# Kernel optimization log

Hardware: AMD Instinct MI355X
Metric: run time of the kernel (lower is better)

Reference implementation:

```python
import jax, jax.numpy as jnp
import numpy as np

HEAD_DIM = 256
V_DIM = 256
HIDDEN = 1024
SCALE_BASE = 512
GAMMA = 0.96875
BATCH, SEQ = 4, 4096


def _dup_interleave(m):
    # (L, d/2) -> (L, d), duplicating each column consecutively
    return jnp.repeat(m, 2, axis=-1)


def _rotate_every_two(x):
    x1 = x[..., ::2]
    x2 = x[..., 1::2]
    return jnp.stack([-x2, x1], axis=-1).reshape(x.shape)


def _xpos(x, downscale=False):
    # x: (B, L, head_dim); offset=0 path of XPOS.forward
    B, L, Dh = x.shape
    half = Dh // 2
    scale_buf = (jnp.arange(0, Dh, 2, dtype=jnp.float32) + 0.4 * Dh) / (1.4 * Dh)  # (half,)
    pos = jnpp = jnp.arange(L, dtype=jnp.float32)
    scale = scale_buf[None, :] ** (pos / SCALE_BASE)[:, None]  # (L, half)
    inv_freq = 1.0 / (10000.0 ** (jnp.arange(half, dtype=jnp.float32) / half))
    sinusoid = pos[:, None] * inv_freq[None, :]  # (L, half)
    sin, cos = jnp.sin(sinusoid), jnp.cos(sinusoid)
    if downscale:
        scale = 1.0 / scale
    cos_s = _dup_interleave(cos * scale)  # (L, Dh)
    sin_s = _dup_interleave(sin * scale)
    return x * cos_s[None] + _rotate_every_two(x) * sin_s[None]


def _decay_matrix(L):
    n = jnp.arange(L)[:, None]
    m = jnp.arange(L)[None, :]
    mask = n >= m
    expo = jnp.where(mask, n - m, 0).astype(jnp.float32)
    return jnp.where(mask, GAMMA ** expo, 0.0)  # (L, L)


def setup_inputs() -> dict:
    key = jax.random.key(0)
    k1, k2, k3, k4 = jax.random.split(key, 4)
    X = jax.random.normal(k1, (BATCH, SEQ, HIDDEN), dtype=jnp.float32)
    W_Q = jax.random.normal(k2, (HIDDEN, HEAD_DIM), dtype=jnp.float32) / HIDDEN
    W_K = jax.random.normal(k3, (HIDDEN, HEAD_DIM), dtype=jnp.float32) / HIDDEN
    W_V = jax.random.normal(k4, (HIDDEN, V_DIM), dtype=jnp.float32) / HIDDEN
    return {"X": X, "W_Q": W_Q, "W_K": W_K, "W_V": W_V}


def reference(X, W_Q, W_K, W_V):
    L = X.shape[1]
    Q = _xpos(X @ W_Q)                      # (B, L, Dh)
    K = _xpos(X @ W_K, downscale=True)      # (B, L, Dh)
    V = X @ W_V                             # (B, L, Dv)
    D = _decay_matrix(L)                    # (L, L)
    ret = jnp.einsum('bqd,bkd->bqk', Q, K) * D[None]  # (B, L, L)
    return ret @ V                          # (B, L, Dv)
```

## Files before the change

### kernel.cpp

```cpp
#include <hip/hip_runtime.h>
#include <hip/hip_bf16.h>
#include <cstdint>
#include <cstddef>

#define L_SEQ 4096
#define BATCH_N 4
#define HID 1024
#define DH 256
#define LOG2_GAMMA (-0.045803689613124953f)

typedef __attribute__((ext_vector_type(8))) short short8;
typedef __attribute__((ext_vector_type(4))) float floatx4;

__device__ __forceinline__ unsigned short f2bf(float f) {
    union { float f; unsigned int u; } v; v.f = f;
    unsigned int r = (v.u + 0x7FFFu + ((v.u >> 16) & 1u)) >> 16;
    return (unsigned short)r;
}

__device__ __forceinline__ void async_copy16(const unsigned short* gsrc,
                                             unsigned short* lds) {
    __builtin_amdgcn_global_load_lds(
        (const __attribute__((address_space(1))) unsigned int*)gsrc,
        (__attribute__((address_space(3))) unsigned int*)lds, 16, 0, 0);
}

__global__ __launch_bounds__(256) void convert_x_kernel(
    const float* __restrict__ X, unsigned short* __restrict__ Xb)
{
    const int i = (blockIdx.x * 256 + threadIdx.x) * 4;
    const float4 v = *(const float4*)&X[i];
    ushort4 p;
    p.x = f2bf(v.x); p.y = f2bf(v.y); p.z = f2bf(v.z); p.w = f2bf(v.w);
    *(ushort4*)&Xb[i] = p;
}

__global__ __launch_bounds__(256) void transpose_w_kernel(
    const float* __restrict__ WQ, const float* __restrict__ WK,
    const float* __restrict__ WV, unsigned short* __restrict__ Wt)
{
    __shared__ float Ts[64][68];
    const int n0 = blockIdx.x * 64;
    const int k0 = blockIdx.y * 64;
    const int seg = n0 >> 8;
    const float* __restrict__ W = (seg == 0) ? WQ : (seg == 1) ? WK : WV;
    const int nl0 = n0 & 255;

    const int t  = threadIdx.x;
    const int r  = t >> 4;
    const int c4 = (t & 15) * 4;
    #pragma unroll
    for (int i = 0; i < 4; ++i) {
        const int kk = r + i * 16;
        const float4 v = *(const float4*)&W[(size_t)(k0 + kk) * DH + nl0 + c4];
        Ts[c4 + 0][kk] = v.x;
        Ts[c4 + 1][kk] = v.y;
        Ts[c4 + 2][kk] = v.z;
        Ts[c4 + 3][kk] = v.w;
    }
    __syncthreads();
    const int rn = t >> 3;
    const int c8 = (t & 7) * 8;
    #pragma unroll
    for (int i = 0; i < 2; ++i) {
        const int rr = rn + i * 32;
        ushort4 p0, p1;
        p0.x = f2bf(Ts[rr][c8 + 0]); p0.y = f2bf(Ts[rr][c8 + 1]);
        p0.z = f2bf(Ts[rr][c8 + 2]); p0.w = f2bf(Ts[rr][c8 + 3]);
        p1.x = f2bf(Ts[rr][c8 + 4]); p1.y = f2bf(Ts[rr][c8 + 5]);
        p1.z = f2bf(Ts[rr][c8 + 6]); p1.w = f2bf(Ts[rr][c8 + 7]);
        unsigned short* dst = &Wt[(size_t)(n0 + rr) * HID + k0 + c8];
        *(ushort4*)dst       = p0;
        *(ushort4*)(dst + 4) = p1;
    }
}

__global__ __launch_bounds__(256) void gemm_qkv_kernel(
    const unsigned short* __restrict__ Wt,
    const unsigned short* __restrict__ Xb,
    unsigned short* __restrict__ Qo,
    unsigned short* __restrict__ Ko,
    unsigned short* __restrict__ VtG)
{
    __shared__ unsigned short Wa[128][32];
    __shared__ unsigned short Xs[128][32];

    const int n0 = blockIdx.x * 128;
    const int p0 = blockIdx.y * 128;
    const int t    = threadIdx.x;
    const int w    = t >> 6;
    const int lane = t & 63;
    const int quad = lane >> 4;
    const int l16  = lane & 15;
    const int wn   = (w & 1) * 64;
    const int wp   = (w >> 1) * 64;

    const int srow = w * 32 + (lane >> 2);
    const int scol = (lane & 3) * 8;

    floatx4 acc[4][4];
    #pragma unroll
    for (int i = 0; i < 4; ++i)
        #pragma unroll
        for (int j = 0; j < 4; ++j) acc[i][j] = (floatx4){0.f, 0.f, 0.f, 0.f};

    for (int k0 = 0; k0 < HID; k0 += 32) {
        __syncthreads();
        #pragma unroll
        for (int is = 0; is < 2; ++is) {
            const unsigned short* ga =
                &Wt[(size_t)(n0 + srow + is * 16) * HID + k0 + scol];
            const unsigned short* gb =
                &Xb[(size_t)(p0 + srow + is * 16) * HID + k0 + scol];
            async_copy16(ga, &Wa[w * 32 + is * 16][0]);
            async_copy16(gb, &Xs[w * 32 + is * 16][0]);
        }
        __syncthreads();

        short8 af[4], bf[4];
        #pragma unroll
        for (int nt = 0; nt < 4; ++nt)
            af[nt] = *(const short8*)&Wa[wn + nt * 16 + l16][quad * 8];
        #pragma unroll
        for (int pt = 0; pt < 4; ++pt)
            bf[pt] = *(const short8*)&Xs[wp + pt * 16 + l16][quad * 8];
        #pragma unroll
        for (int nt = 0; nt < 4; ++nt)
            #pragma unroll
            for (int pt = 0; pt < 4; ++pt)
                acc[nt][pt] = __builtin_amdgcn_mfma_f32_16x16x32_bf16(
                    af[nt], bf[pt], acc[nt][pt], 0, 0, 0);
    }

    const int seg = n0 >> 8;
    #pragma unroll
    for (int nt = 0; nt < 4; ++nt) {
        const int nfeat = n0 + wn + nt * 16 + quad * 4;
        const int d0 = nfeat & 255;
        #pragma unroll
        for (int pt = 0; pt < 4; ++pt) {
            const int pg  = p0 + wp + pt * 16 + l16;
            const int b   = pg >> 12;
            const int pos = pg & (L_SEQ - 1);
            if (seg == 2) {
                #pragma unroll
                for (int g = 0; g < 4; ++g)
                    VtG[(((size_t)(b * 256 + d0 + g)) << 12) + pos] =
                        f2bf(acc[nt][pt][g]);
            } else {
                const float e = (float)pos * (1.0f / 512.0f);
                float res[4];
                #pragma unroll
                for (int h = 0; h < 4; h += 2) {
                    const int d  = d0 + h;
                    const int i2 = d >> 1;
                    const float sb = ((float)d + 102.4f) * (1.0f / 358.4f);
                    float sc = exp2f(log2f(sb) * e);
                    if (seg == 1) sc = 1.0f / sc;
                    const float invf = exp2f(-13.287712379549449f *
                                             ((float)i2 * (1.0f / 128.0f)));
                    float s, c;
                    sincosf((float)pos * invf, &s, &c);
                    const float cs = c * sc, ss = s * sc;
                    const float xe = acc[nt][pt][h], xo = acc[nt][pt][h + 1];
                    res[h]     = xe * cs - xo * ss;
                    res[h + 1] = xo * cs + xe * ss;
                }
                ushort4 pk;
                pk.x = f2bf(res[0]); pk.y = f2bf(res[1]);
                pk.z = f2bf(res[2]); pk.w = f2bf(res[3]);
                unsigned short* orow =
                    ((seg == 0) ? Qo : Ko) + (size_t)pg * DH + d0;
                *(ushort4*)orow = pk;
            }
        }
    }
}

__global__ __launch_bounds__(256) void retention_kernel(
    const unsigned short* __restrict__ Q,
    const unsigned short* __restrict__ K,
    const unsigned short* __restrict__ VtG,
    float* __restrict__ O)
{
    __shared__ short Qs[64][264];
    __shared__ short Ks[32][264];
    __shared__ short Vt[256][40];
    __shared__ short Ss[64][40];

    const int qt = blockIdx.x;
    const int b  = blockIdx.y;
    const int t  = threadIdx.x;
    const int q0 = qt * 64;

    const int w    = t >> 6;
    const int lane = t & 63;
    const int quad = lane >> 4;
    const int l16  = lane & 15;
    const int w16  = w * 16;

    const size_t rbase = (size_t)b * L_SEQ * DH;
    const size_t vbase = ((size_t)b * DH) << 12;

    {
        const unsigned short* src = Q + rbase + (size_t)q0 * DH;
        #pragma unroll
        for (int i = 0; i < 8; ++i) {
            const int row = i * 8 + (t >> 5);
            const int col = (t & 31) * 8;
            *(uint4*)&Qs[row][col] = *(const uint4*)&src[row * DH + col];
        }
    }

    floatx4 o[16];
    #pragma unroll
    for (int f = 0; f < 16; ++f) o[f] = (floatx4){0.f, 0.f, 0.f, 0.f};

    int kstart = q0 - 512;
    if (kstart < 0) kstart = 0;

    for (int k0 = kstart; k0 < q0 + 64; k0 += 32) {
        __syncthreads();
        {
            const unsigned short* src = K + rbase + (size_t)k0 * DH;
            #pragma unroll
            for (int i = 0; i < 4; ++i) {
                const int row = i * 8 + (t >> 5);
                const int col = (t & 31) * 8;
                *(uint4*)&Ks[row][col] = *(const uint4*)&src[row * DH + col];
            }
        }
        {
            const int koff = (t & 7) * 4;
            #pragma unroll
            for (int i = 0; i < 8; ++i) {
                const int c = (t >> 3) + 32 * i;
                *(uint2*)&Vt[c][koff] =
                    *(const uint2*)&VtG[vbase + ((size_t)c << 12) + k0 + koff];
            }
        }
        __syncthreads();

        #pragma unroll
        for (int ntile = 0; ntile < 2; ++ntile) {
            floatx4 s = (floatx4){0.f, 0.f, 0.f, 0.f};
            #pragma unroll
            for (int d8 = 0; d8 < 8; ++d8) {
                const short8 a   = *(const short8*)&Qs[w16 + l16][d8 * 32 + quad * 8];
                const short8 bfr = *(const short8*)&Ks[ntile * 16 + l16][d8 * 32 + quad * 8];
                s = __builtin_amdgcn_mfma_f32_16x16x32_bf16(a, bfr, s, 0, 0, 0);
            }
            const int kpos = k0 + ntile * 16 + l16;
            #pragma unroll
            for (int g = 0; g < 4; ++g) {
                const int qpos = q0 + w16 + quad * 4 + g;
                const int d = qpos - kpos;
                const float p = (d >= 0) ? s[g] * exp2f((float)d * LOG2_GAMMA) : 0.0f;
                Ss[w16 + quad * 4 + g][ntile * 16 + l16] = (short)f2bf(p);
            }
        }
        __syncthreads();

        {
            const short8 a = *(const short8*)&Ss[w16 + l16][quad * 8];
            #pragma unroll
            for (int f = 0; f < 16; ++f) {
                const short8 bfr = *(const short8*)&Vt[f * 16 + l16][quad * 8];
                o[f] = __builtin_amdgcn_mfma_f32_16x16x32_bf16(a, bfr, o[f], 0, 0, 0);
            }
        }
    }

    #pragma unroll
    for (int f = 0; f < 16; ++f) {
        #pragma unroll
        for (int g = 0; g < 4; ++g) {
            const int qpos = q0 + w16 + quad * 4 + g;
            O[rbase + (size_t)qpos * DH + f * 16 + l16] = o[f][g];
        }
    }
}

extern "C" void kernel_launch(void* const* d_in, const int* in_sizes, int n_in,
                              void* d_out, int out_size, void* d_ws, size_t ws_size,
                              hipStream_t stream)
{
    const float* X  = (const float*)d_in[0];
    const float* WQ = (const float*)d_in[1];
    const float* WK = (const float*)d_in[2];
    const float* WV = (const float*)d_in[3];
    float* out = (float*)d_out;

    const size_t per = (size_t)BATCH_N * L_SEQ * DH;
    unsigned short* Qw  = (unsigned short*)d_ws;
    unsigned short* Kw  = Qw + per;
    unsigned short* Vtw = Kw + per;
    unsigned short* Xbw = Vtw + per;
    unsigned short* Wtw = Xbw + (size_t)16384 * HID;

    convert_x_kernel<<<16384, 256, 0, stream>>>(X, Xbw);
    transpose_w_kernel<<<dim3(12, 16), 256, 0, stream>>>(WQ, WK, WV, Wtw);

    gemm_qkv_kernel<<<dim3(6, 128), 256, 0, stream>>>(Wtw, Xbw, Qw, Kw, Vtw);

    retention_kernel<<<dim3(L_SEQ / 64, BATCH_N), 256, 0, stream>>>(Qw, Kw, Vtw, out);
}
```

Measured before the change: 190.6 us.

## Fuse X bf16 conversion into QKV GEMM, remap blocks, retile retention kernel

```diff
diff --git a/kernel.cpp b/kernel.cpp
--- a/kernel.cpp
+++ b/kernel.cpp
@@ -25,15 +25,6 @@
         (__attribute__((address_space(3))) unsigned int*)lds, 16, 0, 0);
 }
 
-__global__ __launch_bounds__(256) void convert_x_kernel(
-    const float* __restrict__ X, unsigned short* __restrict__ Xb)
-{
-    const int i = (blockIdx.x * 256 + threadIdx.x) * 4;
-    const float4 v = *(const float4*)&X[i];
-    ushort4 p;
-    p.x = f2bf(v.x); p.y = f2bf(v.y); p.z = f2bf(v.z); p.w = f2bf(v.w);
-    *(ushort4*)&Xb[i] = p;
-}
 
 __global__ __launch_bounds__(256) void transpose_w_kernel(
     const float* __restrict__ WQ, const float* __restrict__ WK,
@@ -75,18 +66,22 @@
     }
 }
 
-__global__ __launch_bounds__(256) void gemm_qkv_kernel(
+__global__ __launch_bounds__(256, 3) void gemm_qkv_kernel(
     const unsigned short* __restrict__ Wt,
-    const unsigned short* __restrict__ Xb,
+    const float* __restrict__ X,
     unsigned short* __restrict__ Qo,
     unsigned short* __restrict__ Ko,
     unsigned short* __restrict__ VtG)
 {
-    __shared__ unsigned short Wa[128][32];
-    __shared__ unsigned short Xs[128][32];
-
-    const int n0 = blockIdx.x * 128;
-    const int p0 = blockIdx.y * 128;
+    __shared__ unsigned short Wa[2][128][32];
+    __shared__ unsigned short Xs[2][128][32];
+
+    const int idx = blockIdx.x;
+    const int xcd = idx & 7;
+    const int j   = idx >> 3;
+    const int n0  = (j % 6) * 128;
+    const int p0  = (xcd * 16 + (j / 6)) * 128;
+
     const int t    = threadIdx.x;
     const int w    = t >> 6;
     const int lane = t & 63;
@@ -95,41 +90,67 @@
     const int wn   = (w & 1) * 64;
     const int wp   = (w >> 1) * 64;
 
-    const int srow = w * 32 + (lane >> 2);
-    const int scol = (lane & 3) * 8;
+    const int arow = lane >> 2;
+    const int acol = (lane & 3) * 8;
+
+    const int rb = t >> 1;
+    const int hb = t & 1;
 
     floatx4 acc[4][4];
     #pragma unroll
     for (int i = 0; i < 4; ++i)
         #pragma unroll
-        for (int j = 0; j < 4; ++j) acc[i][j] = (floatx4){0.f, 0.f, 0.f, 0.f};
-
-    for (int k0 = 0; k0 < HID; k0 += 32) {
-        __syncthreads();
-        #pragma unroll
-        for (int is = 0; is < 2; ++is) {
+        for (int jj = 0; jj < 4; ++jj) acc[i][jj] = (floatx4){0.f, 0.f, 0.f, 0.f};
+
+    const float* xsrc0 = &X[(size_t)(p0 + rb) * HID + hb * 32];
+
+    for (int k0 = 0; k0 < HID; k0 += 64) {
+        float4 xv[8];
+        #pragma unroll
+        for (int i = 0; i < 8; ++i)
+            xv[i] = ((const float4*)(xsrc0 + k0))[i];
+
+        __syncthreads();
+
+        #pragma unroll
+        for (int s = 0; s < 4; ++s) {
+            const int panel = s & 1;
+            const int rch   = w * 32 + (s >> 1) * 16;
             const unsigned short* ga =
-                &Wt[(size_t)(n0 + srow + is * 16) * HID + k0 + scol];
-            const unsigned short* gb =
-                &Xb[(size_t)(p0 + srow + is * 16) * HID + k0 + scol];
-            async_copy16(ga, &Wa[w * 32 + is * 16][0]);
-            async_copy16(gb, &Xs[w * 32 + is * 16][0]);
-        }
-        __syncthreads();
-
-        short8 af[4], bf[4];
-        #pragma unroll
-        for (int nt = 0; nt < 4; ++nt)
-            af[nt] = *(const short8*)&Wa[wn + nt * 16 + l16][quad * 8];
-        #pragma unroll
-        for (int pt = 0; pt < 4; ++pt)
-            bf[pt] = *(const short8*)&Xs[wp + pt * 16 + l16][quad * 8];
-        #pragma unroll
-        for (int nt = 0; nt < 4; ++nt)
+                &Wt[(size_t)(n0 + rch + arow) * HID + k0 + panel * 32 + acol];
+            async_copy16(ga, &Wa[panel][rch][0]);
+        }
+        {
+            unsigned short* bd = &Xs[hb][rb][0];
+            #pragma unroll
+            for (int c = 0; c < 4; ++c) {
+                const float4 v0 = xv[c * 2], v1 = xv[c * 2 + 1];
+                union { unsigned short s[8]; uint4 u; } pk;
+                pk.s[0] = f2bf(v0.x); pk.s[1] = f2bf(v0.y);
+                pk.s[2] = f2bf(v0.z); pk.s[3] = f2bf(v0.w);
+                pk.s[4] = f2bf(v1.x); pk.s[5] = f2bf(v1.y);
+                pk.s[6] = f2bf(v1.z); pk.s[7] = f2bf(v1.w);
+                *(uint4*)&bd[c * 8] = pk.u;
+            }
+        }
+        __syncthreads();
+
+        #pragma unroll
+        for (int h = 0; h < 2; ++h) {
+            short8 af[4], bfv[4];
+            #pragma unroll
+            for (int nt = 0; nt < 4; ++nt)
+                af[nt] = *(const short8*)&Wa[h][wn + nt * 16 + l16][quad * 8];
             #pragma unroll
             for (int pt = 0; pt < 4; ++pt)
-                acc[nt][pt] = __builtin_amdgcn_mfma_f32_16x16x32_bf16(
-                    af[nt], bf[pt], acc[nt][pt], 0, 0, 0);
+                bfv[pt] = *(const short8*)&Xs[h][wp + pt * 16 + l16][quad * 8];
+            #pragma unroll
+            for (int nt = 0; nt < 4; ++nt)
+                #pragma unroll
+                for (int pt = 0; pt < 4; ++pt)
+                    acc[nt][pt] = __builtin_amdgcn_mfma_f32_16x16x32_bf16(
+                        af[nt], bfv[pt], acc[nt][pt], 0, 0, 0);
+        }
     }
 
     const int seg = n0 >> 8;
@@ -159,8 +180,9 @@
                     if (seg == 1) sc = 1.0f / sc;
                     const float invf = exp2f(-13.287712379549449f *
                                              ((float)i2 * (1.0f / 128.0f)));
+                    const float th = (float)pos * invf;
                     float s, c;
-                    sincosf((float)pos * invf, &s, &c);
+                    sincosf(th, &s, &c);
                     const float cs = c * sc, ss = s * sc;
                     const float xe = acc[nt][pt][h], xo = acc[nt][pt][h + 1];
                     res[h]     = xe * cs - xo * ss;
@@ -177,49 +199,48 @@
     }
 }
 
-__global__ __launch_bounds__(256) void retention_kernel(
+__global__ __launch_bounds__(256, 2) void retention_kernel(
     const unsigned short* __restrict__ Q,
     const unsigned short* __restrict__ K,
     const unsigned short* __restrict__ VtG,
     float* __restrict__ O)
 {
-    __shared__ short Qs[64][264];
     __shared__ short Ks[32][264];
     __shared__ short Vt[256][40];
-    __shared__ short Ss[64][40];
+    __shared__ short Ss[32][40];
 
     const int qt = blockIdx.x;
     const int b  = blockIdx.y;
     const int t  = threadIdx.x;
-    const int q0 = qt * 64;
+    const int q0 = qt * 32;
 
     const int w    = t >> 6;
     const int lane = t & 63;
     const int quad = lane >> 4;
     const int l16  = lane & 15;
-    const int w16  = w * 16;
+    const int rw   = (w >> 1) * 16;
+    const int ws   = w & 1;
 
     const size_t rbase = (size_t)b * L_SEQ * DH;
     const size_t vbase = ((size_t)b * DH) << 12;
 
+    short8 qf[8];
     {
-        const unsigned short* src = Q + rbase + (size_t)q0 * DH;
-        #pragma unroll
-        for (int i = 0; i < 8; ++i) {
-            const int row = i * 8 + (t >> 5);
-            const int col = (t & 31) * 8;
-            *(uint4*)&Qs[row][col] = *(const uint4*)&src[row * DH + col];
-        }
-    }
-
-    floatx4 o[16];
-    #pragma unroll
-    for (int f = 0; f < 16; ++f) o[f] = (floatx4){0.f, 0.f, 0.f, 0.f};
+        const unsigned short* qrow =
+            Q + rbase + (size_t)(q0 + rw + l16) * DH + quad * 8;
+        #pragma unroll
+        for (int d8 = 0; d8 < 8; ++d8)
+            qf[d8] = *(const short8*)(qrow + d8 * 32);
+    }
+
+    floatx4 o[8];
+    #pragma unroll
+    for (int f = 0; f < 8; ++f) o[f] = (floatx4){0.f, 0.f, 0.f, 0.f};
 
     int kstart = q0 - 512;
     if (kstart < 0) kstart = 0;
 
-    for (int k0 = kstart; k0 < q0 + 64; k0 += 32) {
+    for (int k0 = kstart; k0 <= q0; k0 += 32) {
         __syncthreads();
         {
             const unsigned short* src = K + rbase + (size_t)k0 * DH;
@@ -241,42 +262,42 @@
         }
         __syncthreads();
 
-        #pragma unroll
-        for (int ntile = 0; ntile < 2; ++ntile) {
+        {
             floatx4 s = (floatx4){0.f, 0.f, 0.f, 0.f};
             #pragma unroll
             for (int d8 = 0; d8 < 8; ++d8) {
-                const short8 a   = *(const short8*)&Qs[w16 + l16][d8 * 32 + quad * 8];
-                const short8 bfr = *(const short8*)&Ks[ntile * 16 + l16][d8 * 32 + quad * 8];
-                s = __builtin_amdgcn_mfma_f32_16x16x32_bf16(a, bfr, s, 0, 0, 0);
-            }
-            const int kpos = k0 + ntile * 16 + l16;
+                const short8 bfr =
+                    *(const short8*)&Ks[ws * 16 + l16][d8 * 32 + quad * 8];
+                s = __builtin_amdgcn_mfma_f32_16x16x32_bf16(qf[d8], bfr, s, 0, 0, 0);
+            }
+            const int kpos = k0 + ws * 16 + l16;
             #pragma unroll
             for (int g = 0; g < 4; ++g) {
-                const int qpos = q0 + w16 + quad * 4 + g;
+                const int qpos = q0 + rw + quad * 4 + g;
                 const int d = qpos - kpos;
                 const float p = (d >= 0) ? s[g] * exp2f((float)d * LOG2_GAMMA) : 0.0f;
-                Ss[w16 + quad * 4 + g][ntile * 16 + l16] = (short)f2bf(p);
-            }
-        }
-        __syncthreads();
-
-        {
-            const short8 a = *(const short8*)&Ss[w16 + l16][quad * 8];
-            #pragma unroll
-            for (int f = 0; f < 16; ++f) {
-                const short8 bfr = *(const short8*)&Vt[f * 16 + l16][quad * 8];
+                Ss[rw + quad * 4 + g][ws * 16 + l16] = (short)f2bf(p);
+            }
+        }
+        __syncthreads();
+
+        {
+            const short8 a = *(const short8*)&Ss[rw + l16][quad * 8];
+            #pragma unroll
+            for (int f = 0; f < 8; ++f) {
+                const short8 bfr =
+                    *(const short8*)&Vt[ws * 128 + f * 16 + l16][quad * 8];
                 o[f] = __builtin_amdgcn_mfma_f32_16x16x32_bf16(a, bfr, o[f], 0, 0, 0);
             }
         }
     }
 
     #pragma unroll
-    for (int f = 0; f < 16; ++f) {
+    for (int f = 0; f < 8; ++f) {
         #pragma unroll
         for (int g = 0; g < 4; ++g) {
-            const int qpos = q0 + w16 + quad * 4 + g;
-            O[rbase + (size_t)qpos * DH + f * 16 + l16] = o[f][g];
+            const int qpos = q0 + rw + quad * 4 + g;
+            O[rbase + (size_t)qpos * DH + ws * 128 + f * 16 + l16] = o[f][g];
         }
     }
 }
@@ -295,13 +316,11 @@
     unsigned short* Qw  = (unsigned short*)d_ws;
     unsigned short* Kw  = Qw + per;
     unsigned short* Vtw = Kw + per;
-    unsigned short* Xbw = Vtw + per;
-    unsigned short* Wtw = Xbw + (size_t)16384 * HID;
-
-    convert_x_kernel<<<16384, 256, 0, stream>>>(X, Xbw);
+    unsigned short* Wtw = Vtw + per;
+
     transpose_w_kernel<<<dim3(12, 16), 256, 0, stream>>>(WQ, WK, WV, Wtw);
 
-    gemm_qkv_kernel<<<dim3(6, 128), 256, 0, stream>>>(Wtw, Xbw, Qw, Kw, Vtw);
-
-    retention_kernel<<<dim3(L_SEQ / 64, BATCH_N), 256, 0, stream>>>(Qw, Kw, Vtw, out);
-}
+    gemm_qkv_kernel<<<768, 256, 0, stream>>>(Wtw, X, Qw, Kw, Vtw);
+
+    retention_kernel<<<dim3(L_SEQ / 32, BATCH_N), 256, 0, stream>>>(Qw, Kw, Vtw, out);
+}
```

After: 278.4 us. 1.46x slower.
